# Optimization experiments

Measured on AMD Instinct MI355X. Metric: run time of the kernel, lower is better.

The kernel has to match this reference:

```python
import jax, jax.numpy as jnp
import numpy as np

FILTER_LENGTHS = (2, 4)  # from module: self.filter_length = [2, 4]


def _get_conv(signal, b, h, l, d_k, conv, w):
    # signal: [b, h*d_k, l] (raw reshape of [b,h,l,d_k], matching torch .reshape)
    f = max(FILTER_LENGTHS)
    pad = f // 2
    padded = jnp.pad(signal, ((0, 0), (0, 0), (pad, pad)))  # [b, d, l+f]
    # unfold(-1, f, 1)[:, :, :l, :] -> sliding windows, keep first l
    idx = jnp.arange(l)[:, None] + jnp.arange(f)[None, :]  # [l, f]
    seq = padded[:, :, idx]  # [b, d, l, f]
    # dynamic filter-length selection: w_f = filter_lengths * w, pick argmax
    f_s = jnp.asarray(FILTER_LENGTHS, dtype=signal.dtype)
    ind = jnp.argmax(f_s * w)
    chosen_len = jnp.asarray(FILTER_LENGTHS)[ind]
    mask = (jnp.arange(f) < chosen_len).astype(signal.dtype)  # [f]
    seq = seq * mask  # broadcast over [b, d, l, f]
    # depthwise-ish conv via einsum, then raw reshape (b, l, h*d_k) -> (b, h, l, d_k)
    out = jnp.einsum('bdlf,dof->blo', seq, conv)
    return out.reshape(b, h, l, d_k)


def reference(Q, K, V, attn_mask, conv_q, conv_k, w):
    b, h, l, d_k = Q.shape
    Qc = _get_conv(Q.reshape(b, h * d_k, l), b, h, l, d_k, conv_q, w) + Q
    Kc = _get_conv(K.reshape(b, h * d_k, l), b, h, l, d_k, conv_k, w) + K
    scores = jnp.einsum('bhqd,bhkd->bhqk', Qc, Kc) / np.sqrt(d_k).astype(Q.dtype)
    attn = jax.nn.softmax(scores, axis=-1)
    context = jnp.einsum('bhqk,bhkd->bhqd', attn, V)
    return context, attn


def setup_inputs() -> dict:
    key = jax.random.key(0)
    ks = jax.random.split(key, 6)
    b, h, l, d_k = 4, 8, 2048, 64
    d = h * d_k
    f = max(FILTER_LENGTHS)
    return {
        'Q': jax.random.normal(ks[0], (b, h, l, d_k), dtype=jnp.float32),
        'K': jax.random.normal(ks[1], (b, h, l, d_k), dtype=jnp.float32),
        'V': jax.random.normal(ks[2], (b, h, l, d_k), dtype=jnp.float32),
        'attn_mask': jnp.zeros((b, 1, l, l), dtype=bool),  # unused by forward
        'conv_q': jax.random.normal(ks[3], (d, d, f), dtype=jnp.float32),
        'conv_k': jax.random.normal(ks[4], (d, d, f), dtype=jnp.float32),
        'w': jax.random.normal(ks[5], (2,), dtype=jnp.float32),
    }
```

## Files before the change

kernel.cpp:

```cpp
#include <hip/hip_runtime.h>

typedef _Float16 f16;
typedef _Float16 f16x8 __attribute__((ext_vector_type(8)));
typedef float f32x16 __attribute__((ext_vector_type(16)));

#define MFMA32(A, B, C) __builtin_amdgcn_mfma_f32_32x32x16_f16(A, B, C, 0, 0, 0)

constexpr int Bb = 4, Hh = 8, Ll = 2048, Dk = 64, Dm = 512, BH = 32;

constexpr size_t NWF = (size_t)16 * 128 * 64 * 8;
constexpr size_t NAF = (size_t)Bb * 64 * 128 * 64 * 8;
constexpr size_t NFF = (size_t)BH * 64 * 4 * 64 * 8;
constexpr size_t NVF = (size_t)BH * 2 * 128 * 64 * 8;

constexpr size_t OFF_WF = 256;
constexpr size_t OFF_AF = OFF_WF + 4 * NWF * sizeof(f16);
constexpr size_t OFF_FF = OFF_AF + 4 * NAF * sizeof(f16);
constexpr size_t OFF_VF = OFF_FF + 4 * NFF * sizeof(f16);

#define QSCALE 0.1803368801111204f

__global__ void kprep_w(const float* __restrict__ convq, const float* __restrict__ convk,
                        const float* __restrict__ w, int* __restrict__ flag,
                        f16* __restrict__ wfhq, f16* __restrict__ wflq,
                        f16* __restrict__ wfhk, f16* __restrict__ wflk) {
    const int len = (4.f * w[1] > 2.f * w[0]) ? 4 : 2;
    if (blockIdx.x == 0 && blockIdx.y == 0 && threadIdx.x == 0) *flag = len;
    int tid = blockIdx.x * 256 + threadIdx.x;
    int o = tid & 511;
    const float* conv = blockIdx.y ? convk : convq;
    f16* dh = blockIdx.y ? wfhk : wfhq;
    f16* dl = blockIdx.y ? wflk : wflq;
    const float4 v = *(const float4*)(conv + (size_t)tid * 4);
    float vv[4] = {v.x, v.y, v.z, v.w};
    int c = tid >> 9, ob = o >> 5;
#pragma unroll
    for (int f = 0; f < 4; ++f) {
        float x = (f < len) ? vv[f] : 0.f;
        f16 hi = (f16)x;
        f16 lo = (f16)(x - (float)hi);
        int k = (f << 9) + c;
        size_t idx = (((size_t)ob * 128 + (k >> 4)) * 64 + ((k >> 3) & 1) * 32 + (o & 31)) * 8 + (k & 7);
        dh[idx] = hi; dl[idx] = lo;
    }
}

__global__ void kprep_a(const float* __restrict__ Q, const float* __restrict__ K,
                        const int* __restrict__ flag,
                        f16* __restrict__ afhq, f16* __restrict__ aflq,
                        f16* __restrict__ afhk, f16* __restrict__ aflk) {
    __shared__ float tile[64][36];
    int tensor = blockIdx.z, b = blockIdx.y;
    int tb = blockIdx.x >> 5, k16g = blockIdx.x & 31;
    int f = k16g >> 3;
    if (f >= *flag) return;
    int c0 = (k16g * 64) & 511;
    const float* S = (tensor ? K : Q) + (size_t)b * Dm * Ll;
    int tid = threadIdx.x;
    int t0 = tb * 32;
#pragma unroll
    for (int i = 0; i < 9; ++i) {
        int e = i * 256 + tid;
        int row = e / 36, col = e - row * 36;
        int t = t0 - 2 + col;
        tile[row][col] = (t >= 0 && t < Ll) ? S[(size_t)(c0 + row) * Ll + t] : 0.f;
    }
    __syncthreads();
    int sub = tid >> 6, lane = tid & 63;
    int k16 = k16g * 4 + sub;
    int khalf = lane >> 5, lane31 = lane & 31;
    f16x8 hv, lv;
#pragma unroll
    for (int j = 0; j < 8; ++j) {
        int cl = sub * 16 + khalf * 8 + j;
        float x = tile[cl][lane31 + f];
        f16 hi = (f16)x;
        hv[j] = hi; lv[j] = (f16)(x - (float)hi);
    }
    f16* dh = tensor ? afhk : afhq;
    f16* dl = tensor ? aflk : aflq;
    size_t idx = ((((size_t)b * 64 + tb) * 128 + k16) * 64 + lane) * 8;
    *(f16x8*)(dh + idx) = hv;
    *(f16x8*)(dl + idx) = lv;
}

__global__ void kprep_v(const float* __restrict__ V, f16* __restrict__ vf) {
    int bh = blockIdx.y, l0 = blockIdx.x * 128;
    int tid = threadIdx.x;
    const float* src = V + (size_t)bh * Ll * Dk;
#pragma unroll
    for (int s = 0; s < 4; ++s) {
        int g = s * 4 + (tid >> 6);
        int lane = tid & 63;
        int l16s = g >> 1, db = g & 1;
        int khalf = lane >> 5, lane31 = lane & 31;
        int d = db * 32 + lane31;
        f16x8 out;
#pragma unroll
        for (int j = 0; j < 8; ++j) {
            int l = l0 + l16s * 16 + khalf * 8 + j;
            out[j] = (f16)src[(size_t)l * Dk + d];
        }
        size_t idx = ((((size_t)bh * 2 + db) * 128 + (l0 >> 4) + l16s) * 64 + lane) * 8;
        *(f16x8*)(vf + idx) = out;
    }
}

__global__ __launch_bounds__(256, 4) void kconv(
    const float* __restrict__ Q, const float* __restrict__ K, const int* __restrict__ flag,
    const f16* __restrict__ afhq, const f16* __restrict__ aflq,
    const f16* __restrict__ afhk, const f16* __restrict__ aflk,
    const f16* __restrict__ wfhq, const f16* __restrict__ wflq,
    const f16* __restrict__ wfhk, const f16* __restrict__ wflk,
    f16* __restrict__ ffhq, f16* __restrict__ fflq,
    f16* __restrict__ ffhk, f16* __restrict__ fflk) {
    int id = blockIdx.x;
    int xcd = id & 7, oTile = (id >> 3) & 3, gidx = id >> 5;
    int g = gidx * 8 + xcd;
    int tt = g & 31, b = (g >> 5) & 3, tensor = (g >> 7) & 1;
    int wave = threadIdx.x >> 6, lane = threadIdx.x & 63;
    int wn = wave & 1, wm = wave >> 1;
    int lane31 = lane & 31, khalf = lane >> 5;
    const f16* ah = (tensor ? afhk : afhq) + ((size_t)(b * 64 + tt * 2 + wm) * 128) * 512;
    const f16* al = (tensor ? aflk : aflq) + ((size_t)(b * 64 + tt * 2 + wm) * 128) * 512;
    const f16* bhp = (tensor ? wfhk : wfhq) + ((size_t)(oTile * 4 + wn * 2) * 128) * 512;
    const f16* blp = (tensor ? wflk : wflq) + ((size_t)(oTile * 4 + wn * 2) * 128) * 512;
    const float* src = (tensor ? K : Q) + (size_t)b * Hh * Ll * Dk;
    f16* dh = (tensor ? ffhk : ffhq);
    f16* dl = (tensor ? fflk : fflq);
    const float scale = tensor ? 1.f : QSCALE;
    const int klen16 = (*flag) << 5;

    f32x16 acc[2];
#pragma unroll
    for (int j = 0; j < 2; ++j)
#pragma unroll
        for (int r = 0; r < 16; ++r) acc[j][r] = 0.f;

    f16x8 Aah, Aal, Abh[2], Abl[2];
    f16x8 Bah, Bal, Bbh[2], Bbl[2];
    const size_t lo8 = (size_t)lane * 8;

    Aah = *(const f16x8*)(ah + lo8);
    Aal = *(const f16x8*)(al + lo8);
    Abh[0] = *(const f16x8*)(bhp + lo8);
    Abl[0] = *(const f16x8*)(blp + lo8);
    Abh[1] = *(const f16x8*)(bhp + 128 * 512 + lo8);
    Abl[1] = *(const f16x8*)(blp + 128 * 512 + lo8);

    for (int k16 = 0; k16 < klen16; k16 += 2) {
        {
            int kn = k16 + 1 < klen16 ? k16 + 1 : k16;
            size_t o = (size_t)kn * 512 + lo8;
            Bah = *(const f16x8*)(ah + o);
            Bal = *(const f16x8*)(al + o);
            Bbh[0] = *(const f16x8*)(bhp + o);
            Bbl[0] = *(const f16x8*)(blp + o);
            Bbh[1] = *(const f16x8*)(bhp + 128 * 512 + o);
            Bbl[1] = *(const f16x8*)(blp + 128 * 512 + o);
        }
#pragma unroll
        for (int j = 0; j < 2; ++j) {
            acc[j] = MFMA32(Aah, Abh[j], acc[j]);
            acc[j] = MFMA32(Aah, Abl[j], acc[j]);
            acc[j] = MFMA32(Aal, Abh[j], acc[j]);
        }
        {
            int kn = k16 + 2 < klen16 ? k16 + 2 : klen16 - 1;
            size_t o = (size_t)kn * 512 + lo8;
            Aah = *(const f16x8*)(ah + o);
            Aal = *(const f16x8*)(al + o);
            Abh[0] = *(const f16x8*)(bhp + o);
            Abl[0] = *(const f16x8*)(blp + o);
            Abh[1] = *(const f16x8*)(bhp + 128 * 512 + o);
            Abl[1] = *(const f16x8*)(blp + 128 * 512 + o);
        }
#pragma unroll
        for (int j = 0; j < 2; ++j) {
            acc[j] = MFMA32(Bah, Bbh[j], acc[j]);
            acc[j] = MFMA32(Bah, Bbl[j], acc[j]);
            acc[j] = MFMA32(Bal, Bbh[j], acc[j]);
        }
    }
#pragma unroll
    for (int j = 0; j < 2; ++j)
#pragma unroll
        for (int r = 0; r < 16; ++r) {
            int trow = tt * 64 + wm * 32 + (r & 3) + ((r >> 2) << 3) + (khalf << 2);
            int ocol = oTile * 128 + wn * 64 + j * 32 + lane31;
            int h = trow >> 8;
            int l = ((trow & 255) << 3) + (ocol >> 6);
            int d = ocol & 63;
            float v2 = (acc[j][r] + src[((size_t)h * Ll + l) * Dk + d]) * scale;
            f16 hi = (f16)v2;
            f16 lo = (f16)(v2 - (float)hi);
            size_t idx = ((((size_t)(b * 8 + h) * 64 + (l >> 5)) * 4 + (d >> 4)) * 64
                          + ((d >> 3) & 1) * 32 + (l & 31)) * 8 + (d & 7);
            dh[idx] = hi; dl[idx] = lo;
        }
}

__global__ __launch_bounds__(256, 3) void kattn(
    const f16* __restrict__ qfh, const f16* __restrict__ qfl,
    const f16* __restrict__ kfh, const f16* __restrict__ kfl,
    const f16* __restrict__ vf,
    float* __restrict__ ctx_out, float* __restrict__ attn_out) {
    __shared__ float combuf[2][32][64];
    __shared__ __align__(16) f16 ptile[4][32][40];
    int id = blockIdx.x;
    int bh = (id & 7) * 4 + (id >> 8);
    int qt = (id >> 3) & 31;
    int wave = threadIdx.x >> 6, lane = threadIdx.x & 63;
    int qg = wave >> 1, kg = wave & 1;
    int lane31 = lane & 31, khalf = lane >> 5;
    int q0 = qt * 64 + qg * 32;

    f16x8 a_h[4], a_l[4];
    {
        size_t qb = ((size_t)bh * 64 + qt * 2 + qg) * 4;
#pragma unroll
        for (int ks = 0; ks < 4; ++ks) {
            a_h[ks] = *(const f16x8*)(qfh + ((qb + ks) * 64 + lane) * 8);
            a_l[ks] = *(const f16x8*)(qfl + ((qb + ks) * 64 + lane) * 8);
        }
    }
    const f16* kbh = kfh + (size_t)bh * 131072;
    const f16* kbl = kfl + (size_t)bh * 131072;
    const int ch0 = kg * 32, ch1 = ch0 + 32;

    float m[16], s[16];
#pragma unroll
    for (int r = 0; r < 16; ++r) { m[r] = -3.0e38f; s[r] = 0.f; }

    for (int ch = ch0; ch < ch1; ++ch) {
        f32x16 acc;
#pragma unroll
        for (int r = 0; r < 16; ++r) acc[r] = 0.f;
        size_t kb = (size_t)ch * 2048 + lane * 8;
#pragma unroll
        for (int ks = 0; ks < 4; ++ks) {
            f16x8 kh8 = *(const f16x8*)(kbh + kb + ks * 512);
            f16x8 kl8 = *(const f16x8*)(kbl + kb + ks * 512);
            acc = MFMA32(a_h[ks], kh8, acc);
            acc = MFMA32(a_h[ks], kl8, acc);
            acc = MFMA32(a_l[ks], kh8, acc);
        }
#pragma unroll
        for (int r = 0; r < 16; ++r) {
            float v = acc[r];
            float d = v - m[r];
            float e = exp2f(-fabsf(d));
            bool gt = d > 0.f;
            s[r] = gt ? __fmaf_rn(s[r], e, 1.f) : (s[r] + e);
            m[r] = gt ? v : m[r];
        }
    }
#pragma unroll
    for (int r = 0; r < 16; ++r) {
        float mm = m[r], ss = s[r];
#pragma unroll
        for (int off = 1; off < 32; off <<= 1) {
            float mo = __shfl_xor(mm, off, 64);
            float so = __shfl_xor(ss, off, 64);
            float mn = fmaxf(mm, mo);
            ss = ss * exp2f(mm - mn) + so * exp2f(mo - mn);
            mm = mn;
        }
        m[r] = mm; s[r] = ss;
    }
    if (kg == 1) {
#pragma unroll
        for (int r = 0; r < 16; ++r) {
            combuf[qg][r][lane] = m[r];
            combuf[qg][16 + r][lane] = s[r];
        }
    }
    __syncthreads();
    if (kg == 0) {
#pragma unroll
        for (int r = 0; r < 16; ++r) {
            float m1 = combuf[qg][r][lane];
            float s1 = combuf[qg][16 + r][lane];
            float mn = fmaxf(m[r], m1);
            float ss = s[r] * exp2f(m[r] - mn) + s1 * exp2f(m1 - mn);
            m[r] = mn; s[r] = 1.f / ss;
            combuf[qg][r][lane] = mn;
            combuf[qg][16 + r][lane] = s[r];
        }
    }
    __syncthreads();
    if (kg == 1) {
#pragma unroll
        for (int r = 0; r < 16; ++r) {
            m[r] = combuf[qg][r][lane];
            s[r] = combuf[qg][16 + r][lane];
        }
    }

    f32x16 ctx[2];
#pragma unroll
    for (int n = 0; n < 2; ++n)
#pragma unroll
        for (int r = 0; r < 16; ++r) ctx[n][r] = 0.f;

    const size_t rowbase = ((size_t)bh * Ll + q0 + lane31) * Ll;

    for (int ch = ch0; ch < ch1; ++ch) {
        f32x16 acc;
#pragma unroll
        for (int r = 0; r < 16; ++r) acc[r] = 0.f;
        size_t kb = (size_t)ch * 2048 + lane * 8;
#pragma unroll
        for (int ks = 0; ks < 4; ++ks) {
            f16x8 kh8 = *(const f16x8*)(kbh + kb + ks * 512);
            f16x8 kl8 = *(const f16x8*)(kbl + kb + ks * 512);
            acc = MFMA32(a_h[ks], kh8, acc);
            acc = MFMA32(a_h[ks], kl8, acc);
            acc = MFMA32(a_l[ks], kh8, acc);
        }
#pragma unroll
        for (int r = 0; r < 16; ++r) {
            float p = exp2f(acc[r] - m[r]) * s[r];
            int row = (r & 3) + ((r >> 2) << 3) + (khalf << 2);
            ptile[wave][row][lane31] = (f16)p;
        }
        __asm__ volatile("s_waitcnt lgkmcnt(0)" ::: "memory");
#pragma unroll
        for (int ks2 = 0; ks2 < 2; ++ks2) {
            f16x8 pa = *(const f16x8*)&ptile[wave][lane31][ks2 * 16 + khalf * 8];
            float* dst = attn_out + rowbase + ch * 32 + ks2 * 16 + khalf * 8;
            float4 v0 = {(float)pa[0], (float)pa[1], (float)pa[2], (float)pa[3]};
            float4 v1 = {(float)pa[4], (float)pa[5], (float)pa[6], (float)pa[7]};
            *(float4*)dst = v0;
            *(float4*)(dst + 4) = v1;
#pragma unroll
            for (int n = 0; n < 2; ++n) {
                size_t off = ((((size_t)bh * 2 + n) * 128 + ch * 2 + ks2) * 64 + lane) * 8;
                f16x8 vb = *(const f16x8*)(vf + off);
                ctx[n] = MFMA32(pa, vb, ctx[n]);
            }
        }
    }
    __syncthreads();
    if (kg == 1) {
#pragma unroll
        for (int n = 0; n < 2; ++n)
#pragma unroll
            for (int r = 0; r < 16; ++r) combuf[qg][n * 16 + r][lane] = ctx[n][r];
    }
    __syncthreads();
    if (kg == 0) {
#pragma unroll
        for (int n = 0; n < 2; ++n)
#pragma unroll
            for (int r = 0; r < 16; ++r) {
                float v = ctx[n][r] + combuf[qg][n * 16 + r][lane];
                int row = (r & 3) + ((r >> 2) << 3) + (khalf << 2);
                ctx_out[((size_t)bh * Ll + q0 + row) * Dk + n * 32 + lane31] = v;
            }
    }
}

extern "C" void kernel_launch(void* const* d_in, const int* in_sizes, int n_in,
                              void* d_out, int out_size, void* d_ws, size_t ws_size,
                              hipStream_t stream) {
    const float* Q = (const float*)d_in[0];
    const float* K = (const float*)d_in[1];
    const float* V = (const float*)d_in[2];
    const float* convq = (const float*)d_in[4];
    const float* convk = (const float*)d_in[5];
    const float* w = (const float*)d_in[6];

    char* ws = (char*)d_ws;
    int* flag = (int*)ws;
    f16* wfhq = (f16*)(ws + OFF_WF);
    f16* wflq = wfhq + NWF;
    f16* wfhk = wflq + NWF;
    f16* wflk = wfhk + NWF;
    f16* afhq = (f16*)(ws + OFF_AF);
    f16* aflq = afhq + NAF;
    f16* afhk = aflq + NAF;
    f16* aflk = afhk + NAF;
    f16* ffhq = (f16*)(ws + OFF_FF);
    f16* fflq = ffhq + NFF;
    f16* ffhk = fflq + NFF;
    f16* fflk = ffhk + NFF;
    f16* vf = (f16*)(ws + OFF_VF);

    float* ctx_out = (float*)d_out;
    float* attn_out = ctx_out + (size_t)BH * Ll * Dk;

    kprep_w<<<dim3(1024, 2), 256, 0, stream>>>(convq, convk, w, flag, wfhq, wflq, wfhk, wflk);
    kprep_v<<<dim3(16, 32), 256, 0, stream>>>(V, vf);
    kprep_a<<<dim3(2048, 4, 2), 256, 0, stream>>>(Q, K, flag, afhq, aflq, afhk, aflk);
    kconv<<<dim3(1024), 256, 0, stream>>>(Q, K, flag, afhq, aflq, afhk, aflk,
                                          wfhq, wflq, wfhk, wflk, ffhq, fflq, ffhk, fflk);
    kattn<<<dim3(1024), 256, 0, stream>>>(ffhq, fflq, ffhk, fflk, vf, ctx_out, attn_out);
}
```

Baseline: 1.066 ms.

## Restructure conv GEMM with LDS-tiled shifted-window inputs and change attn output writes

```diff
diff --git a/kernel.cpp b/kernel.cpp
--- a/kernel.cpp
+++ b/kernel.cpp
@@ -7,81 +7,79 @@
 #define MFMA32(A, B, C) __builtin_amdgcn_mfma_f32_32x32x16_f16(A, B, C, 0, 0, 0)
 
 constexpr int Bb = 4, Hh = 8, Ll = 2048, Dk = 64, Dm = 512, BH = 32;
-
-constexpr size_t NWF = (size_t)16 * 128 * 64 * 8;
-constexpr size_t NAF = (size_t)Bb * 64 * 128 * 64 * 8;
+constexpr int LP = 2052;
+
+constexpr size_t NW  = (size_t)512 * 2048;
+constexpr size_t NST = (size_t)Bb * LP * 512;
 constexpr size_t NFF = (size_t)BH * 64 * 4 * 64 * 8;
 constexpr size_t NVF = (size_t)BH * 2 * 128 * 64 * 8;
 
-constexpr size_t OFF_WF = 256;
-constexpr size_t OFF_AF = OFF_WF + 4 * NWF * sizeof(f16);
-constexpr size_t OFF_FF = OFF_AF + 4 * NAF * sizeof(f16);
+constexpr size_t OFF_W  = 256;
+constexpr size_t OFF_ST = OFF_W + 4 * NW * sizeof(f16);
+constexpr size_t OFF_FF = OFF_ST + 4 * NST * sizeof(f16);
 constexpr size_t OFF_VF = OFF_FF + 4 * NFF * sizeof(f16);
 
 #define QSCALE 0.1803368801111204f
+
+__device__ __forceinline__ void gload_lds16(const void* g, void* l) {
+    __builtin_amdgcn_global_load_lds((const __attribute__((address_space(1))) unsigned int*)g,
+                                     (__attribute__((address_space(3))) unsigned int*)l, 16, 0, 0);
+}
 
 __global__ void kprep_w(const float* __restrict__ convq, const float* __restrict__ convk,
                         const float* __restrict__ w, int* __restrict__ flag,
-                        f16* __restrict__ wfhq, f16* __restrict__ wflq,
-                        f16* __restrict__ wfhk, f16* __restrict__ wflk) {
+                        f16* __restrict__ wqh, f16* __restrict__ wql,
+                        f16* __restrict__ wkh, f16* __restrict__ wkl) {
     const int len = (4.f * w[1] > 2.f * w[0]) ? 4 : 2;
     if (blockIdx.x == 0 && blockIdx.y == 0 && threadIdx.x == 0) *flag = len;
     int tid = blockIdx.x * 256 + threadIdx.x;
-    int o = tid & 511;
+    int o = tid >> 9, c = tid & 511;
     const float* conv = blockIdx.y ? convk : convq;
-    f16* dh = blockIdx.y ? wfhk : wfhq;
-    f16* dl = blockIdx.y ? wflk : wflq;
-    const float4 v = *(const float4*)(conv + (size_t)tid * 4);
+    f16* dh = blockIdx.y ? wkh : wqh;
+    f16* dl = blockIdx.y ? wkl : wql;
+    const float4 v = *(const float4*)(conv + ((size_t)c * 512 + o) * 4);
     float vv[4] = {v.x, v.y, v.z, v.w};
-    int c = tid >> 9, ob = o >> 5;
 #pragma unroll
     for (int f = 0; f < 4; ++f) {
         float x = (f < len) ? vv[f] : 0.f;
         f16 hi = (f16)x;
         f16 lo = (f16)(x - (float)hi);
-        int k = (f << 9) + c;
-        size_t idx = (((size_t)ob * 128 + (k >> 4)) * 64 + ((k >> 3) & 1) * 32 + (o & 31)) * 8 + (k & 7);
+        size_t idx = (size_t)o * 2048 + (f << 9) + c;
         dh[idx] = hi; dl[idx] = lo;
     }
 }
 
-__global__ void kprep_a(const float* __restrict__ Q, const float* __restrict__ K,
-                        const int* __restrict__ flag,
-                        f16* __restrict__ afhq, f16* __restrict__ aflq,
-                        f16* __restrict__ afhk, f16* __restrict__ aflk) {
-    __shared__ float tile[64][36];
-    int tensor = blockIdx.z, b = blockIdx.y;
-    int tb = blockIdx.x >> 5, k16g = blockIdx.x & 31;
-    int f = k16g >> 3;
-    if (f >= *flag) return;
-    int c0 = (k16g * 64) & 511;
-    const float* S = (tensor ? K : Q) + (size_t)b * Dm * Ll;
-    int tid = threadIdx.x;
-    int t0 = tb * 32;
-#pragma unroll
-    for (int i = 0; i < 9; ++i) {
-        int e = i * 256 + tid;
-        int row = e / 36, col = e - row * 36;
-        int t = t0 - 2 + col;
-        tile[row][col] = (t >= 0 && t < Ll) ? S[(size_t)(c0 + row) * Ll + t] : 0.f;
-    }
-    __syncthreads();
-    int sub = tid >> 6, lane = tid & 63;
-    int k16 = k16g * 4 + sub;
-    int khalf = lane >> 5, lane31 = lane & 31;
-    f16x8 hv, lv;
-#pragma unroll
-    for (int j = 0; j < 8; ++j) {
-        int cl = sub * 16 + khalf * 8 + j;
-        float x = tile[cl][lane31 + f];
-        f16 hi = (f16)x;
-        hv[j] = hi; lv[j] = (f16)(x - (float)hi);
-    }
-    f16* dh = tensor ? afhk : afhq;
-    f16* dl = tensor ? aflk : aflq;
-    size_t idx = ((((size_t)b * 64 + tb) * 128 + k16) * 64 + lane) * 8;
-    *(f16x8*)(dh + idx) = hv;
-    *(f16x8*)(dl + idx) = lv;
+__global__ void kprep_s(const float* __restrict__ Q, const float* __restrict__ K,
+                        f16* __restrict__ stqh, f16* __restrict__ stql,
+                        f16* __restrict__ stkh, f16* __restrict__ stkl) {
+    __shared__ float tile[64][65];
+    int z = blockIdx.z;
+    int tensor = z >> 2, b = z & 3;
+    const float* src = (tensor ? K : Q) + (size_t)b * Dm * Ll;
+    f16* dh = (tensor ? stkh : stqh) + (size_t)b * LP * Dm;
+    f16* dl = (tensor ? stkl : stql) + (size_t)b * LP * Dm;
+    int j0 = blockIdx.x * 64, c0 = blockIdx.y * 64;
+    int tl = threadIdx.x & 63, tg = threadIdx.x >> 6;
+#pragma unroll
+    for (int r = 0; r < 16; ++r) {
+        int cl = (r << 2) + tg;
+        int tabs = j0 + tl - 2;
+        float v = (tabs >= 0 && tabs < Ll) ? src[(size_t)(c0 + cl) * Ll + tabs] : 0.f;
+        tile[cl][tl] = v;
+    }
+    __syncthreads();
+#pragma unroll
+    for (int r = 0; r < 16; ++r) {
+        int jl = (r << 2) + tg;
+        int j = j0 + jl;
+        if (j < LP) {
+            float v = tile[tl][jl];
+            f16 hi = (f16)v;
+            f16 lo = (f16)(v - (float)hi);
+            dh[(size_t)j * Dm + c0 + tl] = hi;
+            dl[(size_t)j * Dm + c0 + tl] = lo;
+        }
+    }
 }
 
 __global__ void kprep_v(const float* __restrict__ V, f16* __restrict__ vf) {
@@ -106,107 +104,108 @@
     }
 }
 
-__global__ __launch_bounds__(256, 4) void kconv(
+__global__ __launch_bounds__(256, 2) void kconv(
     const float* __restrict__ Q, const float* __restrict__ K, const int* __restrict__ flag,
-    const f16* __restrict__ afhq, const f16* __restrict__ aflq,
-    const f16* __restrict__ afhk, const f16* __restrict__ aflk,
-    const f16* __restrict__ wfhq, const f16* __restrict__ wflq,
-    const f16* __restrict__ wfhk, const f16* __restrict__ wflk,
+    const f16* __restrict__ stqh, const f16* __restrict__ stql,
+    const f16* __restrict__ stkh, const f16* __restrict__ stkl,
+    const f16* __restrict__ wqh, const f16* __restrict__ wql,
+    const f16* __restrict__ wkh, const f16* __restrict__ wkl,
     f16* __restrict__ ffhq, f16* __restrict__ fflq,
     f16* __restrict__ ffhk, f16* __restrict__ fflk) {
+    __shared__ f16 At[128 * 64], Bt[128 * 64];
     int id = blockIdx.x;
-    int xcd = id & 7, oTile = (id >> 3) & 3, gidx = id >> 5;
-    int g = gidx * 8 + xcd;
-    int tt = g & 31, b = (g >> 5) & 3, tensor = (g >> 7) & 1;
-    int wave = threadIdx.x >> 6, lane = threadIdx.x & 63;
-    int wn = wave & 1, wm = wave >> 1;
+    int oTile = id & 3, tensor = (id >> 2) & 1;
+    int tt = (id >> 3) & 15, b = (id >> 7) & 3;
+    int tid = threadIdx.x;
+    int wave = tid >> 6, lane = tid & 63;
+    int wm = wave >> 1, wn = wave & 1;
     int lane31 = lane & 31, khalf = lane >> 5;
-    const f16* ah = (tensor ? afhk : afhq) + ((size_t)(b * 64 + tt * 2 + wm) * 128) * 512;
-    const f16* al = (tensor ? aflk : aflq) + ((size_t)(b * 64 + tt * 2 + wm) * 128) * 512;
-    const f16* bhp = (tensor ? wfhk : wfhq) + ((size_t)(oTile * 4 + wn * 2) * 128) * 512;
-    const f16* blp = (tensor ? wflk : wflq) + ((size_t)(oTile * 4 + wn * 2) * 128) * 512;
+    int t0 = tt * 128, o0 = oTile * 128;
+    const f16* sh = (tensor ? stkh : stqh) + (size_t)b * LP * Dm;
+    const f16* sl = (tensor ? stkl : stql) + (size_t)b * LP * Dm;
+    const f16* wh = tensor ? wkh : wqh;
+    const f16* wl = tensor ? wkl : wql;
     const float* src = (tensor ? K : Q) + (size_t)b * Hh * Ll * Dk;
     f16* dh = (tensor ? ffhk : ffhq);
     f16* dl = (tensor ? fflk : fflq);
     const float scale = tensor ? 1.f : QSCALE;
-    const int klen16 = (*flag) << 5;
-
-    f32x16 acc[2];
-#pragma unroll
-    for (int j = 0; j < 2; ++j)
-#pragma unroll
-        for (int r = 0; r < 16; ++r) acc[j][r] = 0.f;
-
-    f16x8 Aah, Aal, Abh[2], Abl[2];
-    f16x8 Bah, Bal, Bbh[2], Bbl[2];
-    const size_t lo8 = (size_t)lane * 8;
-
-    Aah = *(const f16x8*)(ah + lo8);
-    Aal = *(const f16x8*)(al + lo8);
-    Abh[0] = *(const f16x8*)(bhp + lo8);
-    Abl[0] = *(const f16x8*)(blp + lo8);
-    Abh[1] = *(const f16x8*)(bhp + 128 * 512 + lo8);
-    Abl[1] = *(const f16x8*)(blp + 128 * 512 + lo8);
-
-    for (int k16 = 0; k16 < klen16; k16 += 2) {
-        {
-            int kn = k16 + 1 < klen16 ? k16 + 1 : k16;
-            size_t o = (size_t)kn * 512 + lo8;
-            Bah = *(const f16x8*)(ah + o);
-            Bal = *(const f16x8*)(al + o);
-            Bbh[0] = *(const f16x8*)(bhp + o);
-            Bbl[0] = *(const f16x8*)(blp + o);
-            Bbh[1] = *(const f16x8*)(bhp + 128 * 512 + o);
-            Bbl[1] = *(const f16x8*)(blp + 128 * 512 + o);
-        }
-#pragma unroll
-        for (int j = 0; j < 2; ++j) {
-            acc[j] = MFMA32(Aah, Abh[j], acc[j]);
-            acc[j] = MFMA32(Aah, Abl[j], acc[j]);
-            acc[j] = MFMA32(Aal, Abh[j], acc[j]);
-        }
-        {
-            int kn = k16 + 2 < klen16 ? k16 + 2 : klen16 - 1;
-            size_t o = (size_t)kn * 512 + lo8;
-            Aah = *(const f16x8*)(ah + o);
-            Aal = *(const f16x8*)(al + o);
-            Abh[0] = *(const f16x8*)(bhp + o);
-            Abl[0] = *(const f16x8*)(blp + o);
-            Abh[1] = *(const f16x8*)(bhp + 128 * 512 + o);
-            Abl[1] = *(const f16x8*)(blp + 128 * 512 + o);
-        }
-#pragma unroll
-        for (int j = 0; j < 2; ++j) {
-            acc[j] = MFMA32(Bah, Bbh[j], acc[j]);
-            acc[j] = MFMA32(Bah, Bbl[j], acc[j]);
-            acc[j] = MFMA32(Bal, Bbh[j], acc[j]);
-        }
-    }
-#pragma unroll
-    for (int j = 0; j < 2; ++j)
-#pragma unroll
-        for (int r = 0; r < 16; ++r) {
-            int trow = tt * 64 + wm * 32 + (r & 3) + ((r >> 2) << 3) + (khalf << 2);
-            int ocol = oTile * 128 + wn * 64 + j * 32 + lane31;
-            int h = trow >> 8;
-            int l = ((trow & 255) << 3) + (ocol >> 6);
-            int d = ocol & 63;
-            float v2 = (acc[j][r] + src[((size_t)h * Ll + l) * Dk + d]) * scale;
-            f16 hi = (f16)v2;
-            f16 lo = (f16)(v2 - (float)hi);
-            size_t idx = ((((size_t)(b * 8 + h) * 64 + (l >> 5)) * 4 + (d >> 4)) * 64
-                          + ((d >> 3) & 1) * 32 + (l & 31)) * 8 + (d & 7);
-            dh[idx] = hi; dl[idx] = lo;
-        }
-}
-
-__global__ __launch_bounds__(256, 3) void kattn(
+    const int klen = (*flag) << 9;
+    const int iters = (3 * klen) >> 6;
+
+    f32x16 acc[2][2];
+#pragma unroll
+    for (int i = 0; i < 2; ++i)
+#pragma unroll
+        for (int j = 0; j < 2; ++j)
+#pragma unroll
+            for (int r = 0; r < 16; ++r) acc[i][j][r] = 0.f;
+
+    for (int it = 0; it < iters; ++it) {
+        int kp = it << 6;
+        int p = (kp >= 2 * klen) ? 2 : (kp >= klen ? 1 : 0);
+        int k0 = kp - p * klen;
+        int f = k0 >> 9, c0 = k0 & 511;
+        const f16* srcA = (p == 2) ? sl : sh;
+        const f16* srcB = (p == 1) ? wl : wh;
+        __syncthreads();
+#pragma unroll
+        for (int c = 0; c < 4; ++c) {
+            int s = c * 256 + tid;
+            int row = s >> 3;
+            int gk = ((s & 7) ^ (row & 7)) * 8;
+            gload_lds16(srcA + (size_t)(t0 + f + row) * 512 + c0 + gk, &At[s * 8]);
+            gload_lds16(srcB + (size_t)(o0 + row) * 2048 + k0 + gk, &Bt[s * 8]);
+        }
+        __syncthreads();
+#pragma unroll
+        for (int kk = 0; kk < 4; ++kk) {
+            int cc = (kk << 1) + khalf;
+            f16x8 av[2], bv[2];
+#pragma unroll
+            for (int i = 0; i < 2; ++i) {
+                int row = wm * 64 + i * 32 + lane31;
+                av[i] = *(const f16x8*)&At[(row * 8 + (cc ^ (row & 7))) * 8];
+            }
+#pragma unroll
+            for (int j = 0; j < 2; ++j) {
+                int row = wn * 64 + j * 32 + lane31;
+                bv[j] = *(const f16x8*)&Bt[(row * 8 + (cc ^ (row & 7))) * 8];
+            }
+#pragma unroll
+            for (int i = 0; i < 2; ++i)
+#pragma unroll
+                for (int j = 0; j < 2; ++j)
+                    acc[i][j] = MFMA32(av[i], bv[j], acc[i][j]);
+        }
+    }
+#pragma unroll
+    for (int i = 0; i < 2; ++i)
+#pragma unroll
+        for (int j = 0; j < 2; ++j)
+#pragma unroll
+            for (int r = 0; r < 16; ++r) {
+                int trow = t0 + wm * 64 + i * 32 + (r & 3) + ((r >> 2) << 3) + (khalf << 2);
+                int ocol = o0 + wn * 64 + j * 32 + lane31;
+                int h = trow >> 8;
+                int l = ((trow & 255) << 3) + (ocol >> 6);
+                int d = ocol & 63;
+                float v2 = (acc[i][j][r] + src[((size_t)h * Ll + l) * Dk + d]) * scale;
+                f16 hi = (f16)v2;
+                f16 lo = (f16)(v2 - (float)hi);
+                size_t idx = ((((size_t)(b * 8 + h) * 64 + (l >> 5)) * 4 + (d >> 4)) * 64
+                              + ((d >> 3) & 1) * 32 + (l & 31)) * 8 + (d & 7);
+                dh[idx] = hi; dl[idx] = lo;
+            }
+}
+
+__global__ __launch_bounds__(256, 4) void kattn(
     const f16* __restrict__ qfh, const f16* __restrict__ qfl,
     const f16* __restrict__ kfh, const f16* __restrict__ kfl,
     const f16* __restrict__ vf,
     float* __restrict__ ctx_out, float* __restrict__ attn_out) {
-    __shared__ float combuf[2][32][64];
-    __shared__ __align__(16) f16 ptile[4][32][40];
+    __shared__ __align__(16) char smem[16384];
+    float (*combuf)[32][64] = (float (*)[32][64])smem;
+    f16 (*ptile)[32][40] = (f16 (*)[32][40])smem;
     int id = blockIdx.x;
     int bh = (id & 7) * 4 + (id >> 8);
     int qt = (id >> 3) & 31;
@@ -232,6 +231,7 @@
 #pragma unroll
     for (int r = 0; r < 16; ++r) { m[r] = -3.0e38f; s[r] = 0.f; }
 
+#pragma unroll 2
     for (int ch = ch0; ch < ch1; ++ch) {
         f32x16 acc;
 #pragma unroll
@@ -296,6 +296,7 @@
             s[r] = combuf[qg][16 + r][lane];
         }
     }
+    __syncthreads();
 
     f32x16 ctx[2];
 #pragma unroll
@@ -303,7 +304,7 @@
 #pragma unroll
         for (int r = 0; r < 16; ++r) ctx[n][r] = 0.f;
 
-    const size_t rowbase = ((size_t)bh * Ll + q0 + lane31) * Ll;
+    const size_t base_q = ((size_t)bh * Ll + q0) * Ll + lane31;
 
     for (int ch = ch0; ch < ch1; ++ch) {
         f32x16 acc;
@@ -322,17 +323,13 @@
         for (int r = 0; r < 16; ++r) {
             float p = exp2f(acc[r] - m[r]) * s[r];
             int row = (r & 3) + ((r >> 2) << 3) + (khalf << 2);
+            attn_out[base_q + (size_t)row * Ll + ch * 32] = p;
             ptile[wave][row][lane31] = (f16)p;
         }
         __asm__ volatile("s_waitcnt lgkmcnt(0)" ::: "memory");
 #pragma unroll
         for (int ks2 = 0; ks2 < 2; ++ks2) {
             f16x8 pa = *(const f16x8*)&ptile[wave][lane31][ks2 * 16 + khalf * 8];
-            float* dst = attn_out + rowbase + ch * 32 + ks2 * 16 + khalf * 8;
-            float4 v0 = {(float)pa[0], (float)pa[1], (float)pa[2], (float)pa[3]};
-            float4 v1 = {(float)pa[4], (float)pa[5], (float)pa[6], (float)pa[7]};
-            *(float4*)dst = v0;
-            *(float4*)(dst + 4) = v1;
 #pragma unroll
             for (int n = 0; n < 2; ++n) {
                 size_t off = ((((size_t)bh * 2 + n) * 128 + ch * 2 + ks2) * 64 + lane) * 8;
@@ -373,14 +370,14 @@
 
     char* ws = (char*)d_ws;
     int* flag = (int*)ws;
-    f16* wfhq = (f16*)(ws + OFF_WF);
-    f16* wflq = wfhq + NWF;
-    f16* wfhk = wflq + NWF;
-    f16* wflk = wfhk + NWF;
-    f16* afhq = (f16*)(ws + OFF_AF);
-    f16* aflq = afhq + NAF;
-    f16* afhk = aflq + NAF;
-    f16* aflk = afhk + NAF;
+    f16* wqh = (f16*)(ws + OFF_W);
+    f16* wql = wqh + NW;
+    f16* wkh = wql + NW;
+    f16* wkl = wkh + NW;
+    f16* stqh = (f16*)(ws + OFF_ST);
+    f16* stql = stqh + NST;
+    f16* stkh = stql + NST;
+    f16* stkl = stkh + NST;
     f16* ffhq = (f16*)(ws + OFF_FF);
     f16* fflq = ffhq + NFF;
     f16* ffhk = fflq + NFF;
@@ -390,10 +387,10 @@
     float* ctx_out = (float*)d_out;
     float* attn_out = ctx_out + (size_t)BH * Ll * Dk;
 
-    kprep_w<<<dim3(1024, 2), 256, 0, stream>>>(convq, convk, w, flag, wfhq, wflq, wfhk, wflk);
+    kprep_w<<<dim3(1024, 2), 256, 0, stream>>>(convq, convk, w, flag, wqh, wql, wkh, wkl);
+    kprep_s<<<dim3(33, 8, 8), 256, 0, stream>>>(Q, K, stqh, stql, stkh, stkl);
     kprep_v<<<dim3(16, 32), 256, 0, stream>>>(V, vf);
-    kprep_a<<<dim3(2048, 4, 2), 256, 0, stream>>>(Q, K, flag, afhq, aflq, afhk, aflk);
-    kconv<<<dim3(1024), 256, 0, stream>>>(Q, K, flag, afhq, aflq, afhk, aflk,
-                                          wfhq, wflq, wfhk, wflk, ffhq, fflq, ffhk, fflk);
+    kconv<<<dim3(512), 256, 0, stream>>>(Q, K, flag, stqh, stql, stkh, stkl,
+                                         wqh, wql, wkh, wkl, ffhq, fflq, ffhk, fflk);
     kattn<<<dim3(1024), 256, 0, stream>>>(ffhq, fflq, ffhk, fflk, vf, ctx_out, attn_out);
 }
```

Measured after the change: 1.081 ms. About the same (+1.4%).
